# Optimization experiments

Measured on AMD Instinct MI355X. Metric: run time of the kernel, lower is better.

Reference implementation:

```python
import jax, jax.numpy as jnp
import numpy as np

B, S, E2, E = 2, 512, 512, 256  # batch, seq, 2*encode_size, encode_size


def setup_inputs() -> dict:
    key = jax.random.key(0)
    k1, k2, k3, k4 = jax.random.split(key, 4)
    query = jax.random.normal(k1, (B, S, E2), dtype=jnp.float32)
    value = jax.random.normal(k2, (B, S, E2), dtype=jnp.float32)
    # nn.Linear weights (no bias); stored as [in, out] for x @ W convention
    Wd = jax.random.normal(k3, (E2, E), dtype=jnp.float32) * (1.0 / np.sqrt(E2))
    vd = jax.random.normal(k4, (E,), dtype=jnp.float32) * (1.0 / np.sqrt(E))
    return {"query": query, "value": value, "Wd": Wd, "vd": vd}


def reference(query, value, Wd, vd):
    # q = query.unsqueeze(1) -> [B,1,S,2E]; k = query.unsqueeze(2) -> [B,S,1,2E]
    # NOTE: original module ignores its `key` arg; both factors come from query.
    qk = query[:, None, :, :] * query[:, :, None, :]        # [B,S,S,2E]
    h = jnp.tanh(jnp.einsum('bsth,hd->bstd', qk, Wd))        # [B,S,S,E]
    sjt = jnp.einsum('bstd,d->bst', h, vd)                   # [B,S,S]
    atten = jax.nn.softmax(sjt, axis=2)                      # softmax over dim=2
    # dropout p=0.0 -> identity
    context = jnp.einsum('bst,btd->bsd', atten, value)       # bmm
    return (context, atten)
```

## Files before the change

### kernel.cpp

```cpp
#include <hip/hip_runtime.h>

#define B_  2
#define S_  512
#define E2_ 512
#define E_  256

#define TT  64
#define KB  32
#define LDK 40

using f32x4 = __attribute__((ext_vector_type(4))) float;
using f16x8 = __attribute__((ext_vector_type(8))) _Float16;

__device__ __forceinline__ float tanh_fast(float x) {
    float e = __expf(2.0f * x);
    return 1.0f - 2.0f / (e + 1.0f);
}

#define SBAR() __builtin_amdgcn_sched_barrier(0)

__global__ void prep_all(const float* __restrict__ q, _Float16* __restrict__ qh,
                         const float* __restrict__ Wd, _Float16* __restrict__ Wp2) {
    int idx = blockIdx.x * 256 + threadIdx.x;
    float4 v = *(const float4*)(q + idx * 4);
    _Float16 h4[4] = {(_Float16)v.x, (_Float16)v.y, (_Float16)v.z, (_Float16)v.w};
    *(short4*)(qh + idx * 4) = *(short4*)h4;
    int h = idx >> 8;
    int d = idx & 255;
    int ko = h >> 5;
    int kk = h & 31;
    Wp2[ko * (E_ * KB) + d * KB + kk] = (_Float16)Wd[idx];
}

__global__ __launch_bounds__(256, 4)
void stage1(const _Float16* __restrict__ qh,
            const _Float16* __restrict__ Wp2,
            const float* __restrict__ vd,
            float* __restrict__ logits ) {
    const int x  = blockIdx.x;
    const int p  = x >> 6;
    const int sl = x & 63;
    const int b  = blockIdx.y;
    int sj = 0;
    while ((sj + 1) * (sj + 2) / 2 <= p) ++sj;
    const int ti = p - sj * (sj + 1) / 2;
    const int s  = sj * TT + sl;
    const int t0 = ti * TT;

    __shared__ _Float16 sA[2][TT * LDK];
    __shared__ _Float16 sQsh[E2_];
    __shared__ float sVd[E_];

    const int tid = threadIdx.x;
    {
        const _Float16* qsrow = qh + ((size_t)(b * S_ + s)) * E2_;
        sQsh[tid]       = qsrow[tid];
        sQsh[tid + 256] = qsrow[tid + 256];
        sVd[tid & 255]  = vd[tid & 255];
    }
    __syncthreads();

    const int wave = tid >> 6;
    const int lane = tid & 63;
    const int wd   = wave;
    const int l15  = lane & 15;
    const int l4   = lane >> 4;

    const int a_row = tid >> 2;
    const int a_g   = tid & 3;
    const int a_off = a_row * LDK + a_g * 8;
    const _Float16* qt = qh + ((size_t)(b * S_ + t0 + a_row)) * E2_ + a_g * 8;

    const _Float16* wpb = Wp2 + (wd * 64 + l15) * KB + l4 * 8;

    f16x8 ra;
    auto ALOAD  = [&](int k0) { ra = *(const f16x8*)(qt + k0); };
    auto AWRITE = [&](int k0, int hh) {
        f16x8 q = *(const f16x8*)&sQsh[k0 + a_g * 8];
        *(f16x8*)&sA[hh][a_off] = ra * q;
    };

    f32x4 acc[4][4] = {};

    ALOAD(0);
    SBAR();
    AWRITE(0, 0);
    SBAR();
    ALOAD(KB);
    SBAR();
    asm volatile("s_waitcnt lgkmcnt(0)" ::: "memory");
    __builtin_amdgcn_s_barrier();
    SBAR();

    for (int ko = 0; ko < E2_ / KB; ++ko) {
        const int h = ko & 1;
        f16x8 bf[4];
        {
            const _Float16* wk = wpb + ko * (E_ * KB);
#pragma unroll
            for (int fd = 0; fd < 4; ++fd)
                bf[fd] = *(const f16x8*)(wk + fd * 16 * KB);
        }
        SBAR();
        f16x8 af[4];
#pragma unroll
        for (int ft = 0; ft < 4; ++ft) {
            int row = ft * 16 + l15;
            af[ft] = *(const f16x8*)&sA[h][row * LDK + l4 * 8];
        }
        SBAR();
        if (ko < 15) { AWRITE((ko + 1) * KB, h ^ 1); SBAR(); }
        if (ko < 14) { ALOAD((ko + 2) * KB); SBAR(); }
        if (ko < 15) {
            asm volatile("s_waitcnt lgkmcnt(0)" ::: "memory");
            __builtin_amdgcn_s_barrier();
            SBAR();
        }
#pragma unroll
        for (int ft = 0; ft < 4; ++ft)
#pragma unroll
            for (int fd = 0; fd < 4; ++fd)
                acc[ft][fd] = __builtin_amdgcn_mfma_f32_16x16x32_f16(af[ft], bf[fd], acc[ft][fd], 0, 0, 0);
    }

    __syncthreads();

    float* sRed = (float*)&sA[0][0];
    {
        float vdr[4];
#pragma unroll
        for (int fd = 0; fd < 4; ++fd) vdr[fd] = sVd[wd * 64 + fd * 16 + l15];
#pragma unroll
        for (int ft = 0; ft < 4; ++ft) {
#pragma unroll
            for (int r = 0; r < 4; ++r) {
                float pp = 0.f;
#pragma unroll
                for (int fd = 0; fd < 4; ++fd)
                    pp += tanh_fast(acc[ft][fd][r]) * vdr[fd];
                pp += __shfl_xor(pp, 1);
                pp += __shfl_xor(pp, 2);
                pp += __shfl_xor(pp, 4);
                pp += __shfl_xor(pp, 8);
                if (l15 == 0) {
                    int tl = ft * 16 + l4 * 4 + r;
                    sRed[tl * 4 + wd] = pp;
                }
            }
        }
    }
    __syncthreads();
    if (tid < TT) {
        float v = sRed[tid * 4 + 0] + sRed[tid * 4 + 1] + sRed[tid * 4 + 2] + sRed[tid * 4 + 3];
        int t = t0 + tid;
        logits[((size_t)(b * S_ + s)) * S_ + t] = v;
        logits[((size_t)(b * S_ + t)) * S_ + s] = v;
    }
}

__global__ void softmax_k(float* __restrict__ atten) {
    const int row  = blockIdx.x;
    const int lane = threadIdx.x;
    float* p = atten + (size_t)row * S_;
    float4 v0 = *(float4*)(p + lane * 8);
    float4 v1 = *(float4*)(p + lane * 8 + 4);
    float vv[8] = {v0.x, v0.y, v0.z, v0.w, v1.x, v1.y, v1.z, v1.w};
    float m = vv[0];
#pragma unroll
    for (int j = 1; j < 8; ++j) m = fmaxf(m, vv[j]);
#pragma unroll
    for (int off = 1; off < 64; off <<= 1) m = fmaxf(m, __shfl_xor(m, off));
    float ssum = 0.f;
#pragma unroll
    for (int j = 0; j < 8; ++j) { vv[j] = __expf(vv[j] - m); ssum += vv[j]; }
#pragma unroll
    for (int off = 1; off < 64; off <<= 1) ssum += __shfl_xor(ssum, off);
    float inv = 1.0f / ssum;
    float4 o0 = {vv[0] * inv, vv[1] * inv, vv[2] * inv, vv[3] * inv};
    float4 o1 = {vv[4] * inv, vv[5] * inv, vv[6] * inv, vv[7] * inv};
    *(float4*)(p + lane * 8)     = o0;
    *(float4*)(p + lane * 8 + 4) = o1;
}

__global__ __launch_bounds__(256)
void context_k(const float* __restrict__ atten, const float* __restrict__ value,
               float* __restrict__ ctx) {
    __shared__ float sA[32][65];
    __shared__ float sV[64][65];
    const int b  = blockIdx.z;
    const int s0 = blockIdx.y * 32;
    const int e0 = blockIdx.x * 64;
    const int tid = threadIdx.x;
    const int ts = tid >> 4;
    const int te = tid & 15;

    float acc[2][4] = {};
    for (int k0 = 0; k0 < S_; k0 += 64) {
        {
            int r = tid >> 3;
            int c = (tid & 7) * 8;
            const float* ga = atten + ((size_t)(b * S_ + s0 + r)) * S_ + k0 + c;
            *(float4*)&sA[r][c]     = *(const float4*)ga;
            *(float4*)&sA[r][c + 4] = *(const float4*)(ga + 4);
        }
        {
            int r = tid >> 2;
            int c = (tid & 3) * 16;
            const float* gv = value + ((size_t)(b * S_ + k0 + r)) * E2_ + e0 + c;
#pragma unroll
            for (int j = 0; j < 16; j += 4)
                *(float4*)&sV[r][c + j] = *(const float4*)(gv + j);
        }
        __syncthreads();
#pragma unroll 8
        for (int kk = 0; kk < 64; ++kk) {
            float a0 = sA[ts * 2 + 0][kk];
            float a1 = sA[ts * 2 + 1][kk];
#pragma unroll
            for (int j = 0; j < 4; ++j) {
                float vvv = sV[kk][te * 4 + j];
                acc[0][j] += a0 * vvv;
                acc[1][j] += a1 * vvv;
            }
        }
        __syncthreads();
    }
#pragma unroll
    for (int i = 0; i < 2; ++i)
#pragma unroll
        for (int j = 0; j < 4; ++j)
            ctx[((size_t)(b * S_ + s0 + ts * 2 + i)) * E2_ + e0 + te * 4 + j] = acc[i][j];
}

extern "C" void kernel_launch(void* const* d_in, const int* in_sizes, int n_in,
                              void* d_out, int out_size, void* d_ws, size_t ws_size,
                              hipStream_t stream) {
    const float* query = (const float*)d_in[0];
    const float* value = (const float*)d_in[1];
    const float* Wd    = (const float*)d_in[2];
    const float* vd    = (const float*)d_in[3];

    float* out   = (float*)d_out;
    float* ctx   = out;
    float* atten = out + (size_t)B_ * S_ * E2_;

    const size_t need = (size_t)(B_ * S_ * E2_ + 16 * E_ * KB) * sizeof(_Float16);
    _Float16* qh;
    if (ws_size >= need) {
        qh = (_Float16*)d_ws;
    } else {
        qh = (_Float16*)ctx;
    }
    _Float16* wp2 = qh + (size_t)B_ * S_ * E2_;

    prep_all<<<dim3(512), dim3(256), 0, stream>>>(query, qh, Wd, wp2);
    stage1<<<dim3(2304, B_), dim3(256), 0, stream>>>(qh, wp2, vd, atten);
    softmax_k<<<dim3(B_ * S_), dim3(64), 0, stream>>>(atten);
    context_k<<<dim3(E2_ / 64, S_ / 32, B_), dim3(256), 0, stream>>>(atten, value, ctx);
}
```

Measured before the change: 140.3 us.

## Split stage1 across eight waves and double-buffer weight fragment loads

The stage1 block grows from 256 to 512 threads. Each of eight waves now covers 32 output features instead of 64, which halves the accumulator registers per wave. Weight fragments are prefetched one K-step ahead into alternating register buffers, and the scheduling barriers are removed. Only the first four waves stage the A tile, and the logit reduction now sums eight partials. The aim is more waves in flight and better latency hiding, at the cost of more barrier participants and redundant shared A-fragment reads across waves.

New measurement: 152.0 us. +8.4%, slower.

```diff
diff --git a/kernel.cpp b/kernel.cpp
--- a/kernel.cpp
+++ b/kernel.cpp
@@ -16,8 +16,6 @@
     float e = __expf(2.0f * x);
     return 1.0f - 2.0f / (e + 1.0f);
 }
-
-#define SBAR() __builtin_amdgcn_sched_barrier(0)
 
 __global__ void prep_all(const float* __restrict__ q, _Float16* __restrict__ qh,
                          const float* __restrict__ Wd, _Float16* __restrict__ Wp2) {
@@ -32,7 +30,7 @@
     Wp2[ko * (E_ * KB) + d * KB + kk] = (_Float16)Wd[idx];
 }
 
-__global__ __launch_bounds__(256, 4)
+__global__ __launch_bounds__(512, 4)
 void stage1(const _Float16* __restrict__ qh,
             const _Float16* __restrict__ Wp2,
             const float* __restrict__ vd,
@@ -54,9 +52,8 @@
     const int tid = threadIdx.x;
     {
         const _Float16* qsrow = qh + ((size_t)(b * S_ + s)) * E2_;
-        sQsh[tid]       = qsrow[tid];
-        sQsh[tid + 256] = qsrow[tid + 256];
-        sVd[tid & 255]  = vd[tid & 255];
+        sQsh[tid] = qsrow[tid];
+        if (tid < E_) sVd[tid] = vd[tid];
     }
     __syncthreads();
 
@@ -71,7 +68,7 @@
     const int a_off = a_row * LDK + a_g * 8;
     const _Float16* qt = qh + ((size_t)(b * S_ + t0 + a_row)) * E2_ + a_g * 8;
 
-    const _Float16* wpb = Wp2 + (wd * 64 + l15) * KB + l4 * 8;
+    const _Float16* wpb = Wp2 + (wd * 32 + l15) * KB + l4 * 8;
 
     f16x8 ra;
     auto ALOAD  = [&](int k0) { ra = *(const f16x8*)(qt + k0); };
@@ -80,78 +77,84 @@
         *(f16x8*)&sA[hh][a_off] = ra * q;
     };
 
-    f32x4 acc[4][4] = {};
-
-    ALOAD(0);
-    SBAR();
-    AWRITE(0, 0);
-    SBAR();
-    ALOAD(KB);
-    SBAR();
+    f32x4 acc[4][2] = {};
+    f16x8 bf0[2], bf1[2];
+
+#define STEP(KO, BFC, BFN, DOPF)                                                  \
+    {                                                                             \
+        if (DOPF) {           \
+            const _Float16* wn = wpb + ((KO) + 1) * (E_ * KB);                    \
+            BFN[0] = *(const f16x8*)(wn);                                         \
+            BFN[1] = *(const f16x8*)(wn + 16 * KB);                               \
+        }                                                                         \
+        f16x8 af[4];                                                              \
+        _Pragma("unroll")                                                         \
+        for (int ft = 0; ft < 4; ++ft) {                                          \
+            int row = ft * 16 + l15;                                              \
+            af[ft] = *(const f16x8*)&sA[(KO) & 1][row * LDK + l4 * 8];            \
+        }                                                                         \
+        if (wave < 4) {                                                           \
+            if ((KO) < 15) AWRITE(((KO) + 1) * KB, ((KO) & 1) ^ 1);               \
+            if ((KO) < 14) ALOAD(((KO) + 2) * KB);                                \
+        }                                                                         \
+        if ((KO) < 15) {                                                          \
+            asm volatile("s_waitcnt lgkmcnt(0)" ::: "memory");                    \
+            __builtin_amdgcn_s_barrier();                                         \
+        }                                                                         \
+        _Pragma("unroll")                                                         \
+        for (int ft = 0; ft < 4; ++ft)                                            \
+            _Pragma("unroll")                                                     \
+            for (int fd = 0; fd < 2; ++fd)                                        \
+                acc[ft][fd] = __builtin_amdgcn_mfma_f32_16x16x32_f16(             \
+                    af[ft], BFC[fd], acc[ft][fd], 0, 0, 0);                       \
+    }
+
+    if (wave < 4) {
+        ALOAD(0);
+        AWRITE(0, 0);
+        ALOAD(KB);
+    }
+    bf0[0] = *(const f16x8*)(wpb);
+    bf0[1] = *(const f16x8*)(wpb + 16 * KB);
     asm volatile("s_waitcnt lgkmcnt(0)" ::: "memory");
     __builtin_amdgcn_s_barrier();
-    SBAR();
-
-    for (int ko = 0; ko < E2_ / KB; ++ko) {
-        const int h = ko & 1;
-        f16x8 bf[4];
-        {
-            const _Float16* wk = wpb + ko * (E_ * KB);
-#pragma unroll
-            for (int fd = 0; fd < 4; ++fd)
-                bf[fd] = *(const f16x8*)(wk + fd * 16 * KB);
-        }
-        SBAR();
-        f16x8 af[4];
-#pragma unroll
-        for (int ft = 0; ft < 4; ++ft) {
-            int row = ft * 16 + l15;
-            af[ft] = *(const f16x8*)&sA[h][row * LDK + l4 * 8];
-        }
-        SBAR();
-        if (ko < 15) { AWRITE((ko + 1) * KB, h ^ 1); SBAR(); }
-        if (ko < 14) { ALOAD((ko + 2) * KB); SBAR(); }
-        if (ko < 15) {
-            asm volatile("s_waitcnt lgkmcnt(0)" ::: "memory");
-            __builtin_amdgcn_s_barrier();
-            SBAR();
-        }
-#pragma unroll
-        for (int ft = 0; ft < 4; ++ft)
-#pragma unroll
-            for (int fd = 0; fd < 4; ++fd)
-                acc[ft][fd] = __builtin_amdgcn_mfma_f32_16x16x32_f16(af[ft], bf[fd], acc[ft][fd], 0, 0, 0);
-    }
+
+#pragma unroll
+    for (int ko = 0; ko < 16; ko += 2) {
+        STEP(ko,     bf0, bf1, true);
+        STEP(ko + 1, bf1, bf0, (ko + 2) < 16);
+    }
+#undef STEP
 
     __syncthreads();
 
     float* sRed = (float*)&sA[0][0];
     {
-        float vdr[4];
-#pragma unroll
-        for (int fd = 0; fd < 4; ++fd) vdr[fd] = sVd[wd * 64 + fd * 16 + l15];
+        float vdr[2];
+#pragma unroll
+        for (int fd = 0; fd < 2; ++fd) vdr[fd] = sVd[wd * 32 + fd * 16 + l15];
 #pragma unroll
         for (int ft = 0; ft < 4; ++ft) {
 #pragma unroll
             for (int r = 0; r < 4; ++r) {
-                float pp = 0.f;
-#pragma unroll
-                for (int fd = 0; fd < 4; ++fd)
-                    pp += tanh_fast(acc[ft][fd][r]) * vdr[fd];
+                float pp = tanh_fast(acc[ft][0][r]) * vdr[0]
+                         + tanh_fast(acc[ft][1][r]) * vdr[1];
                 pp += __shfl_xor(pp, 1);
                 pp += __shfl_xor(pp, 2);
                 pp += __shfl_xor(pp, 4);
                 pp += __shfl_xor(pp, 8);
                 if (l15 == 0) {
                     int tl = ft * 16 + l4 * 4 + r;
-                    sRed[tl * 4 + wd] = pp;
+                    sRed[tl * 8 + wd] = pp;
                 }
             }
         }
     }
     __syncthreads();
     if (tid < TT) {
-        float v = sRed[tid * 4 + 0] + sRed[tid * 4 + 1] + sRed[tid * 4 + 2] + sRed[tid * 4 + 3];
+        float v = 0.f;
+#pragma unroll
+        for (int j = 0; j < 8; ++j) v += sRed[tid * 8 + j];
         int t = t0 + tid;
         logits[((size_t)(b * S_ + s)) * S_ + t] = v;
         logits[((size_t)(b * S_ + t)) * S_ + s] = v;
@@ -254,7 +257,7 @@
     _Float16* wp2 = qh + (size_t)B_ * S_ * E2_;
 
     prep_all<<<dim3(512), dim3(256), 0, stream>>>(query, qh, Wd, wp2);
-    stage1<<<dim3(2304, B_), dim3(256), 0, stream>>>(qh, wp2, vd, atten);
+    stage1<<<dim3(2304, B_), dim3(512), 0, stream>>>(qh, wp2, vd, atten);
     softmax_k<<<dim3(B_ * S_), dim3(64), 0, stream>>>(atten);
     context_k<<<dim3(E2_ / 64, S_ / 32, B_), dim3(256), 0, stream>>>(atten, value, ctx);
 }
```
